# Kernel optimization log

Hardware: AMD Instinct MI355X
Metric: run time of the kernel (lower is better)

Reference implementation:

```python
import jax, jax.numpy as jnp
import numpy as np

B, S, D = 2, 4096, 1024
H = 16
HD = D // H  # head_dim = 64

def setup_inputs() -> dict:
    key = jax.random.key(0)
    ks = jax.random.split(key, 9)
    sc = 1.0 / np.sqrt(D)
    return {
        "X":   jax.random.normal(ks[0], (B, S, D), dtype=jnp.float32),
        "Wq":  jax.random.normal(ks[1], (D, D), dtype=jnp.float32) * sc,
        "bq":  jax.random.normal(ks[2], (D,), dtype=jnp.float32) * 0.01,
        "Wk":  jax.random.normal(ks[3], (D, D), dtype=jnp.float32) * sc,
        "bk":  jax.random.normal(ks[4], (D,), dtype=jnp.float32) * 0.01,
        "Wv":  jax.random.normal(ks[5], (D, D), dtype=jnp.float32) * sc,
        "bv":  jax.random.normal(ks[6], (D,), dtype=jnp.float32) * 0.01,
        "Wo":  jax.random.normal(ks[7], (D, D), dtype=jnp.float32) * sc,
        "bo":  jax.random.normal(ks[8], (D,), dtype=jnp.float32) * 0.01,
    }

def reference(X, Wq, bq, Wk, bk, Wv, bv, Wo, bo):
    b, s, d = X.shape
    h, hd = H, HD
    # projections
    Q = X @ Wq + bq
    K = X @ Wk + bk
    V = X @ Wv + bv
    # [b, h, s, hd]
    Q = Q.reshape(b, s, h, hd).transpose(0, 2, 1, 3)
    K = K.reshape(b, s, h, hd).transpose(0, 2, 1, 3)
    V = V.reshape(b, s, h, hd).transpose(0, 2, 1, 3)
    scale = 1.0 / jnp.sqrt(jnp.asarray(hd, dtype=X.dtype))  # sqrt(hidden/num_heads)
    scores = jnp.einsum("bhqd,bhkd->bhqk", Q, K) * scale
    attn = jax.nn.softmax(scores, axis=-1)
    out = jnp.einsum("bhqk,bhkd->bhqd", attn, V)
    out = out.transpose(0, 2, 1, 3).reshape(b, s, d)
    return out @ Wo + bo
```

## Files before the change

### kernel.cpp

```cpp
#include <hip/hip_runtime.h>

#define Bsz 2
#define Sq  4096
#define Dm  1024
#define NH  16
#define HD  64

typedef __attribute__((ext_vector_type(8))) short short8;
typedef __attribute__((ext_vector_type(4))) float f32x4;
typedef __attribute__((ext_vector_type(2))) __fp16 fp16x2;
typedef __attribute__((ext_vector_type(4))) _Float16 half4v;

__device__ __forceinline__ unsigned short f2bf(float x) {
    unsigned int u = __float_as_uint(x);
    u += 0x7fffu + ((u >> 16) & 1u);
    return (unsigned short)(u >> 16);
}

__device__ __forceinline__ void gl2lds16(const unsigned short* g, unsigned short* l) {
    __builtin_amdgcn_global_load_lds(
        (const __attribute__((address_space(1))) unsigned int*)g,
        (__attribute__((address_space(3))) unsigned int*)l, 16, 0, 0);
}

__global__ __launch_bounds__(256) void cvt_bf16(const float4* __restrict__ in,
                                                ushort4* __restrict__ out) {
    const int i = blockIdx.x * 256 + threadIdx.x;
    const float4 v = in[i];
    ushort4 r;
    r.x = f2bf(v.x); r.y = f2bf(v.y); r.z = f2bf(v.z); r.w = f2bf(v.w);
    out[i] = r;
}

__global__ __launch_bounds__(256) void wtrans4(const float* __restrict__ Wq,
                                               const float* __restrict__ Wk,
                                               const float* __restrict__ Wv,
                                               const float* __restrict__ Wo,
                                               unsigned short* __restrict__ WtAll) {
    __shared__ float tile[64][65];
    const int z = blockIdx.z;
    const float* W = (z == 0) ? Wq : (z == 1) ? Wk : (z == 2) ? Wv : Wo;
    unsigned short* Wt = WtAll + (size_t)z * Dm * Dm;
    const int k0 = blockIdx.y * 64, n0 = blockIdx.x * 64;
    const int t = threadIdx.x;
    #pragma unroll
    for (int i = 0; i < 16; ++i) {
        const int idx = t + i * 256, r = idx >> 6, c = idx & 63;
        tile[r][c] = W[(size_t)(k0 + r) * Dm + n0 + c];
    }
    __syncthreads();
    #pragma unroll
    for (int i = 0; i < 16; ++i) {
        const int idx = t + i * 256, rr = idx >> 6, cc = idx & 63;
        Wt[(size_t)(n0 + rr) * Dm + k0 + cc] = f2bf(tile[cc][rr]);
    }
}

struct GemmCtx {
    int wm, wn, quad, c16;
    f32x4 acc[4][4];
};

__device__ __forceinline__ void gemm_core(
    const unsigned short* __restrict__ A,
    const unsigned short* __restrict__ Bt,
    int bm, int bn, unsigned short* As, unsigned short* Bs, GemmCtx& cx)
{
    const int t    = threadIdx.x;
    const int w    = t >> 6;
    const int lane = t & 63;
    cx.quad = lane >> 4;
    cx.c16  = lane & 15;
    cx.wm = (w >> 1) * 64;
    cx.wn = (w & 1) * 64;

    #pragma unroll
    for (int i = 0; i < 4; ++i)
        #pragma unroll
        for (int j = 0; j < 4; ++j)
            cx.acc[i][j] = (f32x4){0.f, 0.f, 0.f, 0.f};

    const int srow = lane >> 2, soff = (lane & 3) * 8;
    const unsigned short* Ag0 = A  + (size_t)(bm + w * 16 + srow) * Dm + soff;
    const unsigned short* Ag1 = Ag0 + (size_t)64 * Dm;
    const unsigned short* Bg0 = Bt + (size_t)(bn + w * 16 + srow) * Dm + soff;
    const unsigned short* Bg1 = Bg0 + (size_t)64 * Dm;
    unsigned short* Al0 = As + (w * 16) * 32;
    unsigned short* Al1 = As + (64 + w * 16) * 32;
    unsigned short* Bl0 = Bs + (w * 16) * 32;
    unsigned short* Bl1 = Bs + (64 + w * 16) * 32;

    for (int k0 = 0; k0 < Dm; k0 += 32) {
        __syncthreads();
        gl2lds16(Ag0 + k0, Al0);
        gl2lds16(Ag1 + k0, Al1);
        gl2lds16(Bg0 + k0, Bl0);
        gl2lds16(Bg1 + k0, Bl1);
        __syncthreads();

        short8 af[4], bf[4];
        #pragma unroll
        for (int mt = 0; mt < 4; ++mt)
            af[mt] = *(const short8*)(As + (cx.wm + mt * 16 + cx.c16) * 32 + cx.quad * 8);
        #pragma unroll
        for (int nt = 0; nt < 4; ++nt)
            bf[nt] = *(const short8*)(Bs + (cx.wn + nt * 16 + cx.c16) * 32 + cx.quad * 8);
        #pragma unroll
        for (int mt = 0; mt < 4; ++mt)
            #pragma unroll
            for (int nt = 0; nt < 4; ++nt)
                cx.acc[mt][nt] = __builtin_amdgcn_mfma_f32_16x16x32_bf16(
                    af[mt], bf[nt], cx.acc[mt][nt], 0, 0, 0);
    }
}

__global__ __launch_bounds__(256) void gemm_qkv(
    const unsigned short* __restrict__ A,
    const unsigned short* __restrict__ WtAll,
    const float* __restrict__ bq, const float* __restrict__ bk,
    const float* __restrict__ bv,
    unsigned short* __restrict__ Qh, unsigned short* __restrict__ Kh,
    unsigned short* __restrict__ Vt, float qscale)
{
    __shared__ unsigned short As[128 * 32];
    __shared__ unsigned short Bs[128 * 32];
    const int bm = blockIdx.y * 128;
    const int bn = blockIdx.x * 128;
    GemmCtx cx;
    gemm_core(A, WtAll, bm, bn, As, Bs, cx);

    const int which = bn >> 10;
    const float* bias = (which == 0) ? bq : (which == 1) ? bk : bv;
    const float osc = (which == 0) ? qscale : 1.0f;

    #pragma unroll
    for (int mt = 0; mt < 4; ++mt) {
        const int m0 = bm + cx.wm + mt * 16 + cx.quad * 4;
        #pragma unroll
        for (int nt = 0; nt < 4; ++nt) {
            const int n  = bn + cx.wn + nt * 16 + cx.c16;
            const int nl = n & 1023;
            const float bvv = bias[nl];
            const int h = (nl >> 6), d = nl & 63;
            if (which < 2) {
                unsigned short* C = (which == 0) ? Qh : Kh;
                #pragma unroll
                for (int r = 0; r < 4; ++r) {
                    const int m = m0 + r;
                    const int b = m >> 12, s = m & (Sq - 1);
                    C[((size_t)(b * NH + h) * Sq + s) * HD + d] =
                        f2bf((cx.acc[mt][nt][r] + bvv) * osc);
                }
            } else {
                const int b = m0 >> 12, s0 = m0 & (Sq - 1);
                union { fp16x2 h2[2]; unsigned int u[2]; } pk;
                pk.h2[0] = __builtin_amdgcn_cvt_pkrtz(cx.acc[mt][nt][0] + bvv,
                                                      cx.acc[mt][nt][1] + bvv);
                pk.h2[1] = __builtin_amdgcn_cvt_pkrtz(cx.acc[mt][nt][2] + bvv,
                                                      cx.acc[mt][nt][3] + bvv);
                *(uint2*)(Vt + ((size_t)(b * NH + h) * HD + d) * Sq + s0) =
                    make_uint2(pk.u[0], pk.u[1]);
            }
        }
    }
}

__global__ __launch_bounds__(256) void gemm_o(
    const unsigned short* __restrict__ A,
    const unsigned short* __restrict__ Bt,
    const float* __restrict__ bias, float* __restrict__ C)
{
    __shared__ unsigned short As[128 * 32];
    __shared__ unsigned short Bs[128 * 32];
    const int bm = blockIdx.y * 128;
    const int bn = blockIdx.x * 128;
    GemmCtx cx;
    gemm_core(A, Bt, bm, bn, As, Bs, cx);

    #pragma unroll
    for (int mt = 0; mt < 4; ++mt) {
        const int m0 = bm + cx.wm + mt * 16 + cx.quad * 4;
        #pragma unroll
        for (int nt = 0; nt < 4; ++nt) {
            const int n = bn + cx.wn + nt * 16 + cx.c16;
            const float bvv = bias[n];
            #pragma unroll
            for (int r = 0; r < 4; ++r)
                C[(size_t)(m0 + r) * Dm + n] = cx.acc[mt][nt][r] + bvv;
        }
    }
}

__global__ __launch_bounds__(256, 4) void attn_mfma4(
    const unsigned short* __restrict__ Q,
    const unsigned short* __restrict__ K,
    const unsigned short* __restrict__ Vt,
    unsigned short* __restrict__ AO)
{
    __shared__ unsigned short Ks[2][64 * 72];
    __shared__ unsigned short Vs[2][64 * 72];

    const int qt = blockIdx.x;
    const int bh = blockIdx.y;
    const int b = bh >> 4, h = bh & 15;
    const int t    = threadIdx.x;
    const int w    = t >> 6;
    const int lane = t & 63;
    const int quad = lane >> 4;
    const int c16  = lane & 15;
    const size_t base = (size_t)bh * Sq * HD;

    short8 qf[2][2];
    #pragma unroll
    for (int qg = 0; qg < 2; ++qg) {
        const unsigned short* qp =
            Q + base + (size_t)(qt * 128 + w * 32 + qg * 16 + c16) * HD;
        qf[qg][0] = *(const short8*)(qp + quad * 8);
        qf[qg][1] = *(const short8*)(qp + 32 + quad * 8);
    }

    f32x4 O[2][4];
    f32x4 Lsum[2];
    #pragma unroll
    for (int qg = 0; qg < 2; ++qg) {
        Lsum[qg] = (f32x4){0.f, 0.f, 0.f, 0.f};
        #pragma unroll
        for (int g = 0; g < 4; ++g)
            O[qg][g] = (f32x4){0.f, 0.f, 0.f, 0.f};
    }
    const half4v ones = {(_Float16)1.f, (_Float16)1.f, (_Float16)1.f, (_Float16)1.f};

    const int srow = t >> 2, sc4 = (t & 3) * 8;
    const unsigned short* kg = K  + base + (size_t)srow * HD + sc4;
    const unsigned short* vg = Vt + base + (size_t)srow * Sq + sc4;
    unsigned short* ksl = &Ks[0][0] + srow * 72 + sc4;
    unsigned short* vsl = &Vs[0][0] + srow * 72 + sc4;
    const int LBUF = 64 * 72;

    int4 kr0, kr1, vr0, vr1;
    kr0 = *(const int4*)(kg);
    kr1 = *(const int4*)(kg + 32);
    vr0 = *(const int4*)(vg);
    vr1 = *(const int4*)(vg + 32);
    *(int4*)(ksl)      = kr0;
    *(int4*)(ksl + 32) = kr1;
    *(int4*)(vsl)      = vr0;
    *(int4*)(vsl + 32) = vr1;

    for (int kt = 0; kt < Sq / 64; ++kt) {
        const int cur = kt & 1;
        if (kt + 1 < Sq / 64) {
            const unsigned short* kp = kg + (size_t)(kt + 1) * 64 * HD;
            const unsigned short* vp = vg + (kt + 1) * 64;
            kr0 = *(const int4*)(kp);
            kr1 = *(const int4*)(kp + 32);
            vr0 = *(const int4*)(vp);
            vr1 = *(const int4*)(vp + 32);
        }
        __syncthreads();

        const unsigned short* ksb = &Ks[cur][0];
        const unsigned short* vsb = &Vs[cur][0];

        half4v Pfrag[2][4];
        #pragma unroll
        for (int nt = 0; nt < 4; ++nt) {
            const int krow = nt * 16 + c16;
            const short8 kf0 = *(const short8*)(ksb + krow * 72 + quad * 8);
            const short8 kf1 = *(const short8*)(ksb + krow * 72 + 32 + quad * 8);
            #pragma unroll
            for (int qg = 0; qg < 2; ++qg) {
                f32x4 z = (f32x4){0.f, 0.f, 0.f, 0.f};
                z = __builtin_amdgcn_mfma_f32_16x16x32_bf16(kf0, qf[qg][0], z, 0, 0, 0);
                z = __builtin_amdgcn_mfma_f32_16x16x32_bf16(kf1, qf[qg][1], z, 0, 0, 0);
                const float p0 = __builtin_amdgcn_exp2f(z[0]);
                const float p1 = __builtin_amdgcn_exp2f(z[1]);
                const float p2 = __builtin_amdgcn_exp2f(z[2]);
                const float p3 = __builtin_amdgcn_exp2f(z[3]);
                union { fp16x2 h2[2]; half4v h4; } pk;
                pk.h2[0] = __builtin_amdgcn_cvt_pkrtz(p0, p1);
                pk.h2[1] = __builtin_amdgcn_cvt_pkrtz(p2, p3);
                Pfrag[qg][nt] = pk.h4;
            }
        }

        #pragma unroll
        for (int kk = 0; kk < 4; ++kk) {
            #pragma unroll
            for (int g = 0; g < 4; ++g) {
                const half4v vf = *(const half4v*)
                    (vsb + (g * 16 + c16) * 72 + kk * 16 + quad * 4);
                #pragma unroll
                for (int qg = 0; qg < 2; ++qg)
                    O[qg][g] = __builtin_amdgcn_mfma_f32_16x16x16f16(
                        Pfrag[qg][kk], vf, O[qg][g], 0, 0, 0);
            }
            #pragma unroll
            for (int qg = 0; qg < 2; ++qg)
                Lsum[qg] = __builtin_amdgcn_mfma_f32_16x16x16f16(
                    Pfrag[qg][kk], ones, Lsum[qg], 0, 0, 0);
        }

        if (kt + 1 < Sq / 64) {
            const int nb = cur ^ 1;
            *(int4*)(ksl + nb * LBUF)      = kr0;
            *(int4*)(ksl + nb * LBUF + 32) = kr1;
            *(int4*)(vsl + nb * LBUF)      = vr0;
            *(int4*)(vsl + nb * LBUF + 32) = vr1;
        }
    }

    #pragma unroll
    for (int qg = 0; qg < 2; ++qg) {
        float linv[4];
        #pragma unroll
        for (int r = 0; r < 4; ++r) linv[r] = 1.f / Lsum[qg][r];
        #pragma unroll
        for (int g = 0; g < 4; ++g) {
            const int col = h * HD + g * 16 + c16;
            #pragma unroll
            for (int r = 0; r < 4; ++r) {
                const int s = qt * 128 + w * 32 + qg * 16 + quad * 4 + r;
                AO[((size_t)(b * Sq + s)) * Dm + col] = f2bf(O[qg][g][r] * linv[r]);
            }
        }
    }
}

extern "C" void kernel_launch(void* const* d_in, const int* in_sizes, int n_in,
                              void* d_out, int out_size, void* d_ws, size_t ws_size,
                              hipStream_t stream)
{
    const float* X  = (const float*)d_in[0];
    const float* Wq = (const float*)d_in[1];
    const float* bq = (const float*)d_in[2];
    const float* Wk = (const float*)d_in[3];
    const float* bk = (const float*)d_in[4];
    const float* Wv = (const float*)d_in[5];
    const float* bv = (const float*)d_in[6];
    const float* Wo = (const float*)d_in[7];
    const float* bo = (const float*)d_in[8];
    float* out = (float*)d_out;

    unsigned short* ws = (unsigned short*)d_ws;
    const size_t NX = (size_t)Bsz * Sq * Dm;
    const size_t NW = (size_t)Dm * Dm;
    unsigned short* Xb    = ws; ws += NX;
    unsigned short* WtAll = ws; ws += 4 * NW;
    unsigned short* Qh    = ws; ws += NX;
    unsigned short* Kh    = ws; ws += NX;
    unsigned short* Vt    = ws; ws += NX;
    unsigned short* AO    = ws; ws += NX;

    cvt_bf16<<<(int)(NX / 1024), 256, 0, stream>>>((const float4*)X, (ushort4*)Xb);
    wtrans4<<<dim3(16, 16, 4), 256, 0, stream>>>(Wq, Wk, Wv, Wo, WtAll);

    const float SCL = 0.18033688011112042f;
    gemm_qkv<<<dim3(3 * Dm / 128, (Bsz * Sq) / 128), 256, 0, stream>>>(
        Xb, WtAll, bq, bk, bv, Qh, Kh, Vt, SCL);

    attn_mfma4<<<dim3(Sq / 128, Bsz * NH), 256, 0, stream>>>(Qh, Kh, Vt, AO);

    gemm_o<<<dim3(Dm / 128, (Bsz * Sq) / 128), 256, 0, stream>>>(
        AO, WtAll + 3 * NW, bo, out);
}
```

Baseline: 373.6 us.

## Double attention query tile per block and use 16x16x32 f16 MFMA for PV

The attention kernel now processes 256 queries per block (64 per wave) instead of 128, so each K/V tile loaded into LDS is reused across twice as many queries and half as many blocks stream K/V. The PV and row-sum products switch from 16x16x16 to 16x16x32 f16 MFMA, which requires permuting V columns when writing to LDS so that the concatenated P fragments match the wider K dimension. This raises register pressure (launch bounds lowered to 2 blocks/CU) and halves the grid to 512 blocks, which may reduce latency hiding.

Result: faster. 323.2 us (-13.5%).

```diff
diff --git a/kernel.cpp b/kernel.cpp
--- a/kernel.cpp
+++ b/kernel.cpp
@@ -10,6 +10,7 @@
 typedef __attribute__((ext_vector_type(4))) float f32x4;
 typedef __attribute__((ext_vector_type(2))) __fp16 fp16x2;
 typedef __attribute__((ext_vector_type(4))) _Float16 half4v;
+typedef __attribute__((ext_vector_type(8))) _Float16 half8v;
 
 __device__ __forceinline__ unsigned short f2bf(float x) {
     unsigned int u = __float_as_uint(x);
@@ -191,7 +192,7 @@
     }
 }
 
-__global__ __launch_bounds__(256, 4) void attn_mfma4(
+__global__ __launch_bounds__(256, 2) void attn_mfma5(
     const unsigned short* __restrict__ Q,
     const unsigned short* __restrict__ K,
     const unsigned short* __restrict__ Vt,
@@ -210,31 +211,36 @@
     const int c16  = lane & 15;
     const size_t base = (size_t)bh * Sq * HD;
 
-    short8 qf[2][2];
-    #pragma unroll
-    for (int qg = 0; qg < 2; ++qg) {
+    short8 qf[4][2];
+    #pragma unroll
+    for (int qg = 0; qg < 4; ++qg) {
         const unsigned short* qp =
-            Q + base + (size_t)(qt * 128 + w * 32 + qg * 16 + c16) * HD;
+            Q + base + (size_t)(qt * 256 + w * 64 + qg * 16 + c16) * HD;
         qf[qg][0] = *(const short8*)(qp + quad * 8);
         qf[qg][1] = *(const short8*)(qp + 32 + quad * 8);
     }
 
-    f32x4 O[2][4];
-    f32x4 Lsum[2];
-    #pragma unroll
-    for (int qg = 0; qg < 2; ++qg) {
+    f32x4 O[4][4];
+    f32x4 Lsum[4];
+    #pragma unroll
+    for (int qg = 0; qg < 4; ++qg) {
         Lsum[qg] = (f32x4){0.f, 0.f, 0.f, 0.f};
         #pragma unroll
         for (int g = 0; g < 4; ++g)
             O[qg][g] = (f32x4){0.f, 0.f, 0.f, 0.f};
     }
-    const half4v ones = {(_Float16)1.f, (_Float16)1.f, (_Float16)1.f, (_Float16)1.f};
+    half8v ones8;
+    #pragma unroll
+    for (int i = 0; i < 8; ++i) ones8[i] = (_Float16)1.f;
 
     const int srow = t >> 2, sc4 = (t & 3) * 8;
+    const int f0 = (sc4 < 16) ? sc4 * 2 : (sc4 - 16) * 2 + 4;
+    const int f1 = (sc4 + 4 < 16) ? (sc4 + 4) * 2 : (sc4 - 12) * 2 + 4;
+
     const unsigned short* kg = K  + base + (size_t)srow * HD + sc4;
     const unsigned short* vg = Vt + base + (size_t)srow * Sq + sc4;
     unsigned short* ksl = &Ks[0][0] + srow * 72 + sc4;
-    unsigned short* vsl = &Vs[0][0] + srow * 72 + sc4;
+    unsigned short* vsl = &Vs[0][0] + srow * 72;
     const int LBUF = 64 * 72;
 
     int4 kr0, kr1, vr0, vr1;
@@ -244,8 +250,10 @@
     vr1 = *(const int4*)(vg + 32);
     *(int4*)(ksl)      = kr0;
     *(int4*)(ksl + 32) = kr1;
-    *(int4*)(vsl)      = vr0;
-    *(int4*)(vsl + 32) = vr1;
+    *(uint2*)(vsl + f0)      = make_uint2(vr0.x, vr0.y);
+    *(uint2*)(vsl + f1)      = make_uint2(vr0.z, vr0.w);
+    *(uint2*)(vsl + 32 + f0) = make_uint2(vr1.x, vr1.y);
+    *(uint2*)(vsl + 32 + f1) = make_uint2(vr1.z, vr1.w);
 
     for (int kt = 0; kt < Sq / 64; ++kt) {
         const int cur = kt & 1;
@@ -262,14 +270,14 @@
         const unsigned short* ksb = &Ks[cur][0];
         const unsigned short* vsb = &Vs[cur][0];
 
-        half4v Pfrag[2][4];
+        half4v P4[4][4];
         #pragma unroll
         for (int nt = 0; nt < 4; ++nt) {
             const int krow = nt * 16 + c16;
             const short8 kf0 = *(const short8*)(ksb + krow * 72 + quad * 8);
             const short8 kf1 = *(const short8*)(ksb + krow * 72 + 32 + quad * 8);
             #pragma unroll
-            for (int qg = 0; qg < 2; ++qg) {
+            for (int qg = 0; qg < 4; ++qg) {
                 f32x4 z = (f32x4){0.f, 0.f, 0.f, 0.f};
                 z = __builtin_amdgcn_mfma_f32_16x16x32_bf16(kf0, qf[qg][0], z, 0, 0, 0);
                 z = __builtin_amdgcn_mfma_f32_16x16x32_bf16(kf1, qf[qg][1], z, 0, 0, 0);
@@ -280,38 +288,53 @@
                 union { fp16x2 h2[2]; half4v h4; } pk;
                 pk.h2[0] = __builtin_amdgcn_cvt_pkrtz(p0, p1);
                 pk.h2[1] = __builtin_amdgcn_cvt_pkrtz(p2, p3);
-                Pfrag[qg][nt] = pk.h4;
-            }
-        }
-
-        #pragma unroll
-        for (int kk = 0; kk < 4; ++kk) {
+                P4[qg][nt] = pk.h4;
+            }
+        }
+
+        half8v P32[4][2];
+        #pragma unroll
+        for (int qg = 0; qg < 4; ++qg) {
+            #pragma unroll
+            for (int cc = 0; cc < 2; ++cc) {
+                union { half4v h4[2]; half8v h8; } u;
+                u.h4[0] = P4[qg][2 * cc];
+                u.h4[1] = P4[qg][2 * cc + 1];
+                P32[qg][cc] = u.h8;
+            }
+        }
+
+        #pragma unroll
+        for (int cc = 0; cc < 2; ++cc) {
             #pragma unroll
             for (int g = 0; g < 4; ++g) {
-                const half4v vf = *(const half4v*)
-                    (vsb + (g * 16 + c16) * 72 + kk * 16 + quad * 4);
+                const half8v vf = *(const half8v*)
+                    (vsb + (g * 16 + c16) * 72 + cc * 32 + quad * 8);
                 #pragma unroll
-                for (int qg = 0; qg < 2; ++qg)
-                    O[qg][g] = __builtin_amdgcn_mfma_f32_16x16x16f16(
-                        Pfrag[qg][kk], vf, O[qg][g], 0, 0, 0);
-            }
-            #pragma unroll
-            for (int qg = 0; qg < 2; ++qg)
-                Lsum[qg] = __builtin_amdgcn_mfma_f32_16x16x16f16(
-                    Pfrag[qg][kk], ones, Lsum[qg], 0, 0, 0);
+                for (int qg = 0; qg < 4; ++qg)
+                    O[qg][g] = __builtin_amdgcn_mfma_f32_16x16x32_f16(
+                        P32[qg][cc], vf, O[qg][g], 0, 0, 0);
+            }
+            #pragma unroll
+            for (int qg = 0; qg < 4; ++qg)
+                Lsum[qg] = __builtin_amdgcn_mfma_f32_16x16x32_f16(
+                    P32[qg][cc], ones8, Lsum[qg], 0, 0, 0);
         }
 
         if (kt + 1 < Sq / 64) {
             const int nb = cur ^ 1;
             *(int4*)(ksl + nb * LBUF)      = kr0;
             *(int4*)(ksl + nb * LBUF + 32) = kr1;
-            *(int4*)(vsl + nb * LBUF)      = vr0;
-            *(int4*)(vsl + nb * LBUF + 32) = vr1;
-        }
-    }
-
-    #pragma unroll
-    for (int qg = 0; qg < 2; ++qg) {
+            unsigned short* vdst = vsl + nb * LBUF;
+            *(uint2*)(vdst + f0)      = make_uint2(vr0.x, vr0.y);
+            *(uint2*)(vdst + f1)      = make_uint2(vr0.z, vr0.w);
+            *(uint2*)(vdst + 32 + f0) = make_uint2(vr1.x, vr1.y);
+            *(uint2*)(vdst + 32 + f1) = make_uint2(vr1.z, vr1.w);
+        }
+    }
+
+    #pragma unroll
+    for (int qg = 0; qg < 4; ++qg) {
         float linv[4];
         #pragma unroll
         for (int r = 0; r < 4; ++r) linv[r] = 1.f / Lsum[qg][r];
@@ -320,7 +343,7 @@
             const int col = h * HD + g * 16 + c16;
             #pragma unroll
             for (int r = 0; r < 4; ++r) {
-                const int s = qt * 128 + w * 32 + qg * 16 + quad * 4 + r;
+                const int s = qt * 256 + w * 64 + qg * 16 + quad * 4 + r;
                 AO[((size_t)(b * Sq + s)) * Dm + col] = f2bf(O[qg][g][r] * linv[r]);
             }
         }
@@ -359,7 +382,7 @@
     gemm_qkv<<<dim3(3 * Dm / 128, (Bsz * Sq) / 128), 256, 0, stream>>>(
         Xb, WtAll, bq, bk, bv, Qh, Kh, Vt, SCL);
 
-    attn_mfma4<<<dim3(Sq / 128, Bsz * NH), 256, 0, stream>>>(Qh, Kh, Vt, AO);
+    attn_mfma5<<<dim3(Sq / 256, Bsz * NH), 256, 0, stream>>>(Qh, Kh, Vt, AO);
 
     gemm_o<<<dim3(Dm / 128, (Bsz * Sq) / 128), 256, 0, stream>>>(
         AO, WtAll + 3 * NW, bo, out);
```
